# Kernel optimization log

Measured on AMD Instinct MI355X. Metric: run time of the kernel, lower is better.

The kernel has to match this reference:

```python
import jax, jax.numpy as jnp
import numpy as np

SCALE = 28.0
ALPHA = 0.6
BETA = 0.4
SCALE_POS = 10.0
SCALE_NEG = 40.0
NUM_CLASSES = 11003
FEATURE_SIZE = 2048
BATCH = 1024


def setup_inputs() -> dict:
    key = jax.random.key(0)
    k1, k2, k3, k4 = jax.random.split(key, 4)
    visual_embed = jax.random.normal(k1, (BATCH, FEATURE_SIZE), dtype=jnp.float32)
    textual_embed = jax.random.normal(k2, (BATCH, FEATURE_SIZE), dtype=jnp.float32)
    labels = jax.random.randint(k3, (BATCH,), 0, NUM_CLASSES, dtype=jnp.int64)
    W = jax.random.normal(k4, (FEATURE_SIZE, NUM_CLASSES), dtype=jnp.float32)
    return {"visual_embed": visual_embed, "textual_embed": textual_embed,
            "labels": labels, "W": W}


def _l2norm(x, axis):
    return x / jnp.linalg.norm(x, axis=axis, keepdims=True)


def _cross_entropy(logits, labels):
    logp = jax.nn.log_softmax(logits, axis=-1)
    return -jnp.take_along_axis(logp, labels[:, None], axis=-1).mean()


def reference(visual_embed, textual_embed, labels, W):
    b = visual_embed.shape[0]
    v = _l2norm(visual_embed, 1)
    t = _l2norm(textual_embed, 1)

    # instance loss: scaled cosine classifier + CE on both modalities
    Wn = _l2norm(W, 0)
    v_logits = SCALE * (v @ Wn)
    t_logits = SCALE * (t @ Wn)
    instance_loss = _cross_entropy(v_logits, labels) + _cross_entropy(t_logits, labels)

    # global align loss: masked soft-margin over full BxB similarity.
    # Original loops rows i and columns i, so every entry is counted twice.
    sim = v @ t.T  # [B, B]
    pos_mask = (labels[:, None] == labels[None, :]).astype(sim.dtype)
    loss_pos = jax.nn.softplus(-SCALE_POS * (sim - ALPHA))
    loss_neg = jax.nn.softplus(SCALE_NEG * (sim - BETA))
    per_pair = pos_mask * loss_pos + (1.0 - pos_mask) * loss_neg
    global_align_loss = 2.0 * per_pair.sum() / b

    return jnp.stack([instance_loss, global_align_loss])
```

## Files before the change

### kernel.cpp

```cpp
#include <hip/hip_runtime.h>
#include <hip/hip_bf16.h>
#include <math.h>

#define BATCH 1024
#define FEAT  2048
#define NCLS  11003
#define NPAD  11008
#define NT1   86
#define NPART (NT1 * 2)
#define M1    2048
#define C_SCALE  28.0f
#define C_ALPHA  0.6f
#define C_BETA   0.4f
#define C_SPOS   10.0f
#define C_SNEG   40.0f
#define XSCALE   16.0f
#define SCL1     (C_SCALE / XSCALE)
#define SIMSCL   (1.0f / (XSCALE * XSCALE))
#define SCALE1   0x7F7F7F7F

typedef float floatx4 __attribute__((ext_vector_type(4)));
typedef float f32x16  __attribute__((ext_vector_type(16)));
typedef int   v8i     __attribute__((ext_vector_type(8)));
typedef unsigned char u8;

#define O_ALIGN  ((size_t)0)
#define O_INST   ((size_t)64)
#define O_FIN    ((size_t)128)
#define O_COLSQ  ((size_t)256)
#define O_XN     ((size_t)44288)
#define O_WT     ((size_t)4238592)
#define O_PSUM   ((size_t)26782976)
#define O_LL     ((size_t)28192000)

#define PREP_WBLOCKS (43 * 32)
#define PREP_TOTAL   (PREP_WBLOCKS + M1)

#define MERGE_BLOCKS 256
#define ROWS_PER_MB  (M1 / MERGE_BLOCKS)

__device__ inline float softplusf(float x) {
    return (x > 20.f) ? x : log1pf(expf(x));
}

__device__ inline void gll16(const void* g, void* l) {
    __builtin_amdgcn_global_load_lds(
        (const __attribute__((address_space(1))) unsigned int*)g,
        (__attribute__((address_space(3))) unsigned int*)l, 16, 0, 0);
}

__device__ inline unsigned int pack4_fp8(float a, float b, float c, float d) {
    unsigned int p = __builtin_amdgcn_cvt_pk_fp8_f32(a, b, 0, false);
    p = __builtin_amdgcn_cvt_pk_fp8_f32(c, d, p, true);
    return p;
}

__device__ inline int swz(int c) { return c ^ ((c >> 4) & 7); }

__global__ __launch_bounds__(256) void k_prep(const float* __restrict__ vis,
                                              const float* __restrict__ txt,
                                              const float* __restrict__ W,
                                              u8* __restrict__ Xn,
                                              u8* __restrict__ WT,
                                              float* __restrict__ colsq) {
    __shared__ u8 tileT[1024 * 16];
    __shared__ float cps[4][256];
    __shared__ float sb[256];
    int t = threadIdx.x;
    if (blockIdx.x < PREP_WBLOCKS) {
        int c0 = (blockIdx.x % 43) * 256, f0 = (blockIdx.x / 43) * 64;
        int w = t >> 6, l = t & 63;
        int cbase = c0 + 4 * l;
        unsigned int chunks[4][4];
        float ssq0 = 0.f, ssq1 = 0.f, ssq2 = 0.f, ssq3 = 0.f;
        #pragma unroll
        for (int q = 0; q < 4; ++q) {
            float4 row[4];
            #pragma unroll
            for (int rr = 0; rr < 4; ++rr) {
                int f = f0 + w * 16 + q * 4 + rr;
                const float* p = W + (size_t)f * NCLS + cbase;
                float4 v;
                if (cbase + 3 < NCLS) {
                    __builtin_memcpy(&v, p, 16);
                } else {
                    v.x = (cbase + 0 < NCLS) ? p[0] : 0.f;
                    v.y = (cbase + 1 < NCLS) ? p[1] : 0.f;
                    v.z = (cbase + 2 < NCLS) ? p[2] : 0.f;
                    v.w = (cbase + 3 < NCLS) ? p[3] : 0.f;
                }
                row[rr] = v;
            }
            chunks[0][q] = pack4_fp8(row[0].x, row[1].x, row[2].x, row[3].x);
            chunks[1][q] = pack4_fp8(row[0].y, row[1].y, row[2].y, row[3].y);
            chunks[2][q] = pack4_fp8(row[0].z, row[1].z, row[2].z, row[3].z);
            chunks[3][q] = pack4_fp8(row[0].w, row[1].w, row[2].w, row[3].w);
            #pragma unroll
            for (int rr = 0; rr < 4; ++rr) {
                ssq0 += row[rr].x * row[rr].x;
                ssq1 += row[rr].y * row[rr].y;
                ssq2 += row[rr].z * row[rr].z;
                ssq3 += row[rr].w * row[rr].w;
            }
        }
        #pragma unroll
        for (int j = 0; j < 4; ++j) {
            int L = (4 * l + j) * 4 + w;
            int P = L ^ ((L >> 4) & 7);
            *(uint4*)(tileT + P * 16) =
                make_uint4(chunks[j][0], chunks[j][1], chunks[j][2], chunks[j][3]);
        }
        *(float4*)&cps[w][4 * l] = make_float4(ssq0, ssq1, ssq2, ssq3);
        __syncthreads();
        int c = c0 + t;
        uint4 och[4];
        #pragma unroll
        for (int w2 = 0; w2 < 4; ++w2) {
            int L = t * 4 + w2;
            int P = L ^ ((L >> 4) & 7);
            och[w2] = *(const uint4*)(tileT + P * 16);
        }
        uint4* dst = (uint4*)(WT + (size_t)c * FEAT + f0);
        dst[0] = och[0]; dst[1] = och[1]; dst[2] = och[2]; dst[3] = och[3];
        float s = cps[0][t] + cps[1][t] + cps[2][t] + cps[3][t];
        if (c < NCLS) atomicAdd(&colsq[c], s);
    } else {
        int r = blockIdx.x - PREP_WBLOCKS;
        const float* src = (r < BATCH) ? (vis + (size_t)r * FEAT)
                                       : (txt + (size_t)(r - BATCH) * FEAT);
        float4 x0 = ((const float4*)src)[t];
        float4 x1 = ((const float4*)src)[t + 256];
        float ss = x0.x*x0.x + x0.y*x0.y + x0.z*x0.z + x0.w*x0.w
                 + x1.x*x1.x + x1.y*x1.y + x1.z*x1.z + x1.w*x1.w;
        sb[t] = ss; __syncthreads();
        for (int s = 128; s > 0; s >>= 1) { if (t < s) sb[t] += sb[t + s]; __syncthreads(); }
        float rn = rsqrtf(sb[0]) * XSCALE;
        unsigned int* dst = (unsigned int*)(Xn + (size_t)r * FEAT);
        dst[t]       = pack4_fp8(x0.x*rn, x0.y*rn, x0.z*rn, x0.w*rn);
        dst[t + 256] = pack4_fp8(x1.x*rn, x1.y*rn, x1.z*rn, x1.w*rn);
    }
}

__global__ __launch_bounds__(256, 3) void k_gemm(const u8* __restrict__ Xn,
                                              const u8* __restrict__ WT,
                                              const float* __restrict__ colsq,
                                              const int* __restrict__ labels,
                                              float* __restrict__ psum,
                                              float* __restrict__ ll,
                                              float* __restrict__ align_sum) {
    __shared__ u8 As[128 * 128], Bs[128 * 128];
    f32x16 acc[2][2] = {};
    const int t = threadIdx.x;
    const bool is_sim = (blockIdx.y >= NT1);
    int m0, n0;
    const u8 *A, *B;
    if (!is_sim) {
        m0 = blockIdx.x * 128; n0 = blockIdx.y * 128;
        A = Xn; B = WT;
    } else {
        int s = (blockIdx.y - NT1) * 16 + blockIdx.x;
        m0 = (s >> 3) * 128; n0 = (s & 7) * 128;
        A = Xn; B = Xn + (size_t)BATCH * FEAT;
    }
    const u8 *Ag[4], *Bg[4];
    u8 *lA[4], *lB[4];
    #pragma unroll
    for (int q = 0; q < 4; ++q) {
        int P = q * 256 + t;
        int L = swz(P);
        int r = L >> 3, h = L & 7;
        Ag[q] = A + (size_t)(m0 + r) * FEAT + h * 16;
        Bg[q] = B + (size_t)(n0 + r) * FEAT + h * 16;
        lA[q] = As + P * 16;
        lB[q] = Bs + P * 16;
    }

    const int wave = t >> 6, lane = t & 63;
    const int wm = wave >> 1, wn = wave & 1;
    const int l32 = lane & 31, kh = lane >> 5;
    const uint4* Ard[2][2][2]; const uint4* Brd[2][2][2];
    #pragma unroll
    for (int i = 0; i < 2; ++i)
        #pragma unroll
        for (int ks = 0; ks < 2; ++ks)
            #pragma unroll
            for (int cc = 0; cc < 2; ++cc) {
                int ca = (wm*64 + i*32 + l32) * 8 + ks*4 + kh*2 + cc;
                int cb = (wn*64 + i*32 + l32) * 8 + ks*4 + kh*2 + cc;
                Ard[i][ks][cc] = (const uint4*)(As + swz(ca) * 16);
                Brd[i][ks][cc] = (const uint4*)(Bs + swz(cb) * 16);
            }

    for (int kt = 0; kt < FEAT / 128; ++kt) {
        __syncthreads();
        #pragma unroll
        for (int q = 0; q < 4; ++q) {
            gll16(Ag[q], lA[q]);
            gll16(Bg[q], lB[q]);
        }
        #pragma unroll
        for (int q = 0; q < 4; ++q) { Ag[q] += 128; Bg[q] += 128; }
        __syncthreads();
        #pragma unroll
        for (int ks = 0; ks < 2; ++ks) {
            v8i a[2], b[2];
            #pragma unroll
            for (int i = 0; i < 2; ++i) {
                ((uint4*)&a[i])[0] = *Ard[i][ks][0];
                ((uint4*)&a[i])[1] = *Ard[i][ks][1];
                ((uint4*)&b[i])[0] = *Brd[i][ks][0];
                ((uint4*)&b[i])[1] = *Brd[i][ks][1];
            }
            #pragma unroll
            for (int i = 0; i < 2; ++i)
                #pragma unroll
                for (int j = 0; j < 2; ++j)
                    acc[i][j] = __builtin_amdgcn_mfma_scale_f32_32x32x64_f8f6f4(
                        a[i], b[j], acc[i][j], 0, 0, 0, SCALE1, 0, SCALE1);
        }
    }

    if (!is_sim) {
        float rcol[2]; bool val[2]; int ncol[2];
        #pragma unroll
        for (int j = 0; j < 2; ++j) {
            ncol[j] = n0 + wn*64 + j*32 + l32;
            val[j] = (ncol[j] < NCLS);
            rcol[j] = val[j] ? (SCL1 * rsqrtf(colsq[ncol[j]])) : 0.f;
        }
        const int pidx = blockIdx.y * 2 + wn;
        #pragma unroll
        for (int i = 0; i < 2; ++i) {
            #pragma unroll
            for (int reg = 0; reg < 16; ++reg) {
                int m = m0 + wm*64 + i*32 + (reg & 3) + 8*(reg >> 2) + 4*kh;
                int lm = labels[m & (BATCH - 1)];
                float s = 0.f;
                #pragma unroll
                for (int j = 0; j < 2; ++j) {
                    if (val[j]) {
                        float v = acc[i][j][reg] * rcol[j];
                        if (ncol[j] == lm) ll[m] = v;
                        s += __expf(v - C_SCALE);
                    }
                }
                #pragma unroll
                for (int off = 1; off < 32; off <<= 1) s += __shfl_xor(s, off);
                if (l32 == 0) psum[(size_t)m * NPART + pidx] = s;
            }
        }
    } else {
        int ln[2];
        #pragma unroll
        for (int j = 0; j < 2; ++j) ln[j] = labels[n0 + wn*64 + j*32 + l32];
        float tot = 0.f;
        #pragma unroll
        for (int i = 0; i < 2; ++i) {
            #pragma unroll
            for (int reg = 0; reg < 16; ++reg) {
                int m = m0 + wm*64 + i*32 + (reg & 3) + 8*(reg >> 2) + 4*kh;
                int lm = labels[m];
                #pragma unroll
                for (int j = 0; j < 2; ++j) {
                    float s = acc[i][j][reg] * SIMSCL;
                    float arg = (lm == ln[j]) ? (-C_SPOS * (s - C_ALPHA))
                                              : ( C_SNEG * (s - C_BETA));
                    tot += softplusf(arg);
                }
            }
        }
        #pragma unroll
        for (int off = 1; off < 64; off <<= 1) tot += __shfl_xor(tot, off);
        if (lane == 0) atomicAdd(align_sum, tot);
    }
}

__global__ __launch_bounds__(256) void k_merge(const float* __restrict__ psum,
                                               const float* __restrict__ ll,
                                               float* __restrict__ inst_sum,
                                               const float* __restrict__ align_sum,
                                               int* __restrict__ fin,
                                               float* __restrict__ out) {
    const int t = threadIdx.x;
    const int g = t >> 5, l = t & 31;
    const int r = blockIdx.x * ROWS_PER_MB + g;
    const float* pr = psum + (size_t)r * NPART;
    float s = 0.f;
    for (int p = l; p < NPART; p += 32) s += pr[p];
    #pragma unroll
    for (int off = 1; off < 32; off <<= 1) s += __shfl_xor(s, off);
    __shared__ float sb[ROWS_PER_MB];
    if (l == 0) sb[g] = C_SCALE + logf(s) - ll[r];
    __syncthreads();
    if (t == 0) {
        float ce = 0.f;
        #pragma unroll
        for (int i = 0; i < ROWS_PER_MB; ++i) ce += sb[i];
        atomicAdd(inst_sum, ce);
        __threadfence();
        if (atomicAdd(fin, 1) == MERGE_BLOCKS - 1) {
            __threadfence();
            float is = atomicAdd(inst_sum, 0.f);
            float as = atomicAdd((float*)align_sum, 0.f);
            out[0] = is / (float)BATCH;
            out[1] = as * 2.f / (float)BATCH;
        }
    }
}

extern "C" void kernel_launch(void* const* d_in, const int* in_sizes, int n_in,
                              void* d_out, int out_size, void* d_ws, size_t ws_size,
                              hipStream_t stream) {
    const float* vis    = (const float*)d_in[0];
    const float* txt    = (const float*)d_in[1];
    const int*   labels = (const int*)  d_in[2];
    const float* W      = (const float*)d_in[3];
    float* out = (float*)d_out;
    char*  ws  = (char*)d_ws;

    float* align_sum = (float*)(ws + O_ALIGN);
    float* inst_sum  = (float*)(ws + O_INST);
    int*   fin       = (int*)  (ws + O_FIN);
    float* colsq     = (float*)(ws + O_COLSQ);
    u8* Xn = (u8*)(ws + O_XN);
    u8* WT = (u8*)(ws + O_WT);
    float* psum = (float*)(ws + O_PSUM);
    float* ll   = (float*)(ws + O_LL);

    hipMemsetAsync(ws, 0, O_XN, stream);

    k_prep <<<dim3(PREP_TOTAL), 256, 0, stream>>>(vis, txt, W, Xn, WT, colsq);
    k_gemm <<<dim3(M1 / 128, NT1 + 4), 256, 0, stream>>>(Xn, WT, colsq, labels,
                                                         psum, ll, align_sum);
    k_merge<<<dim3(MERGE_BLOCKS), 256, 0, stream>>>(psum, ll, inst_sum, align_sum,
                                                    fin, out);
}
```

Baseline: 247.6 us.

## Enlarge GEMM block tile to 256x128 with 1x4 warp layout

Changes the fp8 GEMM block tile from 128x128 to 256x128, with each of the four waves owning 64 rows across all 128 columns (2x4 MFMA tiles per wave). This raises arithmetic intensity per LDS load and halves the number of B-tile reloads per row. The partial-sum layout shrinks to one partition per column tile, and the grid is halved. In exchange it uses more LDS and accumulator registers, lowers the occupancy target to 2 blocks per CU, and produces fewer blocks (8x90), which may leave CUs underfilled.

```diff
diff --git a/kernel.cpp b/kernel.cpp
--- a/kernel.cpp
+++ b/kernel.cpp
@@ -7,7 +7,7 @@
 #define NCLS  11003
 #define NPAD  11008
 #define NT1   86
-#define NPART (NT1 * 2)
+#define NPART NT1
 #define M1    2048
 #define C_SCALE  28.0f
 #define C_ALPHA  0.6f
@@ -141,103 +141,116 @@
     }
 }
 
-__global__ __launch_bounds__(256, 3) void k_gemm(const u8* __restrict__ Xn,
+__global__ __launch_bounds__(256, 2) void k_gemm(const u8* __restrict__ Xn,
                                               const u8* __restrict__ WT,
                                               const float* __restrict__ colsq,
                                               const int* __restrict__ labels,
                                               float* __restrict__ psum,
                                               float* __restrict__ ll,
                                               float* __restrict__ align_sum) {
-    __shared__ u8 As[128 * 128], Bs[128 * 128];
-    f32x16 acc[2][2] = {};
+    __shared__ u8 As[256 * 128], Bs[128 * 128];
+    f32x16 acc[2][4] = {};
     const int t = threadIdx.x;
     const bool is_sim = (blockIdx.y >= NT1);
     int m0, n0;
     const u8 *A, *B;
     if (!is_sim) {
-        m0 = blockIdx.x * 128; n0 = blockIdx.y * 128;
+        m0 = blockIdx.x * 256; n0 = blockIdx.y * 128;
         A = Xn; B = WT;
     } else {
-        int s = (blockIdx.y - NT1) * 16 + blockIdx.x;
-        m0 = (s >> 3) * 128; n0 = (s & 7) * 128;
+        int s = (blockIdx.y - NT1) * 8 + blockIdx.x;
+        m0 = (s >> 3) * 256; n0 = (s & 7) * 128;
         A = Xn; B = Xn + (size_t)BATCH * FEAT;
     }
-    const u8 *Ag[4], *Bg[4];
-    u8 *lA[4], *lB[4];
+    const u8 *Ag[8], *Bg[4];
+    u8 *lA[8], *lB[4];
+    #pragma unroll
+    for (int q = 0; q < 8; ++q) {
+        int P = q * 256 + t;
+        int L = swz(P);
+        int r = L >> 3, h = L & 7;
+        Ag[q] = A + (size_t)(m0 + r) * FEAT + h * 16;
+        lA[q] = As + P * 16;
+    }
     #pragma unroll
     for (int q = 0; q < 4; ++q) {
         int P = q * 256 + t;
         int L = swz(P);
         int r = L >> 3, h = L & 7;
-        Ag[q] = A + (size_t)(m0 + r) * FEAT + h * 16;
         Bg[q] = B + (size_t)(n0 + r) * FEAT + h * 16;
-        lA[q] = As + P * 16;
         lB[q] = Bs + P * 16;
     }
 
     const int wave = t >> 6, lane = t & 63;
-    const int wm = wave >> 1, wn = wave & 1;
     const int l32 = lane & 31, kh = lane >> 5;
-    const uint4* Ard[2][2][2]; const uint4* Brd[2][2][2];
+    const uint4* Ard[2][2][2]; const uint4* Brd[4][2][2];
     #pragma unroll
-    for (int i = 0; i < 2; ++i)
-        #pragma unroll
-        for (int ks = 0; ks < 2; ++ks)
-            #pragma unroll
-            for (int cc = 0; cc < 2; ++cc) {
-                int ca = (wm*64 + i*32 + l32) * 8 + ks*4 + kh*2 + cc;
-                int cb = (wn*64 + i*32 + l32) * 8 + ks*4 + kh*2 + cc;
+    for (int ks = 0; ks < 2; ++ks)
+        #pragma unroll
+        for (int cc = 0; cc < 2; ++cc) {
+            #pragma unroll
+            for (int i = 0; i < 2; ++i) {
+                int ca = (wave*64 + i*32 + l32) * 8 + ks*4 + kh*2 + cc;
                 Ard[i][ks][cc] = (const uint4*)(As + swz(ca) * 16);
-                Brd[i][ks][cc] = (const uint4*)(Bs + swz(cb) * 16);
-            }
+            }
+            #pragma unroll
+            for (int j = 0; j < 4; ++j) {
+                int cb = (j*32 + l32) * 8 + ks*4 + kh*2 + cc;
+                Brd[j][ks][cc] = (const uint4*)(Bs + swz(cb) * 16);
+            }
+        }
 
     for (int kt = 0; kt < FEAT / 128; ++kt) {
         __syncthreads();
         #pragma unroll
-        for (int q = 0; q < 4; ++q) {
-            gll16(Ag[q], lA[q]);
-            gll16(Bg[q], lB[q]);
-        }
-        #pragma unroll
-        for (int q = 0; q < 4; ++q) { Ag[q] += 128; Bg[q] += 128; }
+        for (int q = 0; q < 8; ++q) gll16(Ag[q], lA[q]);
+        #pragma unroll
+        for (int q = 0; q < 4; ++q) gll16(Bg[q], lB[q]);
+        #pragma unroll
+        for (int q = 0; q < 8; ++q) Ag[q] += 128;
+        #pragma unroll
+        for (int q = 0; q < 4; ++q) Bg[q] += 128;
         __syncthreads();
         #pragma unroll
         for (int ks = 0; ks < 2; ++ks) {
-            v8i a[2], b[2];
+            v8i a[2], b[4];
             #pragma unroll
             for (int i = 0; i < 2; ++i) {
                 ((uint4*)&a[i])[0] = *Ard[i][ks][0];
                 ((uint4*)&a[i])[1] = *Ard[i][ks][1];
-                ((uint4*)&b[i])[0] = *Brd[i][ks][0];
-                ((uint4*)&b[i])[1] = *Brd[i][ks][1];
+            }
+            #pragma unroll
+            for (int j = 0; j < 4; ++j) {
+                ((uint4*)&b[j])[0] = *Brd[j][ks][0];
+                ((uint4*)&b[j])[1] = *Brd[j][ks][1];
             }
             #pragma unroll
             for (int i = 0; i < 2; ++i)
                 #pragma unroll
-                for (int j = 0; j < 2; ++j)
+                for (int j = 0; j < 4; ++j)
                     acc[i][j] = __builtin_amdgcn_mfma_scale_f32_32x32x64_f8f6f4(
                         a[i], b[j], acc[i][j], 0, 0, 0, SCALE1, 0, SCALE1);
         }
     }
 
     if (!is_sim) {
-        float rcol[2]; bool val[2]; int ncol[2];
-        #pragma unroll
-        for (int j = 0; j < 2; ++j) {
-            ncol[j] = n0 + wn*64 + j*32 + l32;
+        float rcol[4]; bool val[4]; int ncol[4];
+        #pragma unroll
+        for (int j = 0; j < 4; ++j) {
+            ncol[j] = n0 + j*32 + l32;
             val[j] = (ncol[j] < NCLS);
             rcol[j] = val[j] ? (SCL1 * rsqrtf(colsq[ncol[j]])) : 0.f;
         }
-        const int pidx = blockIdx.y * 2 + wn;
+        const int pidx = blockIdx.y;
         #pragma unroll
         for (int i = 0; i < 2; ++i) {
             #pragma unroll
             for (int reg = 0; reg < 16; ++reg) {
-                int m = m0 + wm*64 + i*32 + (reg & 3) + 8*(reg >> 2) + 4*kh;
+                int m = m0 + wave*64 + i*32 + (reg & 3) + 8*(reg >> 2) + 4*kh;
                 int lm = labels[m & (BATCH - 1)];
                 float s = 0.f;
                 #pragma unroll
-                for (int j = 0; j < 2; ++j) {
+                for (int j = 0; j < 4; ++j) {
                     if (val[j]) {
                         float v = acc[i][j][reg] * rcol[j];
                         if (ncol[j] == lm) ll[m] = v;
@@ -250,18 +263,18 @@
             }
         }
     } else {
-        int ln[2];
-        #pragma unroll
-        for (int j = 0; j < 2; ++j) ln[j] = labels[n0 + wn*64 + j*32 + l32];
+        int ln[4];
+        #pragma unroll
+        for (int j = 0; j < 4; ++j) ln[j] = labels[n0 + j*32 + l32];
         float tot = 0.f;
         #pragma unroll
         for (int i = 0; i < 2; ++i) {
             #pragma unroll
             for (int reg = 0; reg < 16; ++reg) {
-                int m = m0 + wm*64 + i*32 + (reg & 3) + 8*(reg >> 2) + 4*kh;
+                int m = m0 + wave*64 + i*32 + (reg & 3) + 8*(reg >> 2) + 4*kh;
                 int lm = labels[m];
                 #pragma unroll
-                for (int j = 0; j < 2; ++j) {
+                for (int j = 0; j < 4; ++j) {
                     float s = acc[i][j][reg] * SIMSCL;
                     float arg = (lm == ln[j]) ? (-C_SPOS * (s - C_ALPHA))
                                               : ( C_SNEG * (s - C_BETA));
@@ -330,8 +343,8 @@
     hipMemsetAsync(ws, 0, O_XN, stream);
 
     k_prep <<<dim3(PREP_TOTAL), 256, 0, stream>>>(vis, txt, W, Xn, WT, colsq);
-    k_gemm <<<dim3(M1 / 128, NT1 + 4), 256, 0, stream>>>(Xn, WT, colsq, labels,
-                                                         psum, ll, align_sum);
+    k_gemm <<<dim3(8, NT1 + 4), 256, 0, stream>>>(Xn, WT, colsq, labels,
+                                                  psum, ll, align_sum);
     k_merge<<<dim3(MERGE_BLOCKS), 256, 0, stream>>>(psum, ll, inst_sum, align_sum,
                                                     fin, out);
 }
```

Result: slower. 276.6 us (+11.7%).
